# Kernel tuning notes

Hardware: AMD Instinct MI355X
Metric: run time of the kernel (lower is better)

Reference implementation:

```python
import jax, jax.numpy as jnp
import numpy as np

D_MODEL = 1024
N_HEADS = 16
D_HEAD = D_MODEL // N_HEADS


def setup_inputs() -> dict:
    key = jax.random.key(0)
    k1, k2, k3 = jax.random.split(key, 3)
    x = jax.random.normal(k1, (2, 2048, D_MODEL), dtype=jnp.float32)
    # torch Linear weights transposed to [in, out] for x @ W
    w_qkv = jax.random.normal(k2, (D_MODEL, 3 * D_MODEL), dtype=jnp.float32) * (D_MODEL ** -0.5)
    w_proj = jax.random.normal(k3, (D_MODEL, D_MODEL), dtype=jnp.float32) * (D_MODEL ** -0.5)
    return {"x": x, "w_qkv": w_qkv, "w_proj": w_proj}


def reference(x, w_qkv, w_proj):
    B, N, D = x.shape
    qkv = x @ w_qkv                              # [B, N, 3D]
    q, k, v = jnp.split(qkv, 3, axis=-1)         # each [B, N, D]

    def split_heads(t):
        return t.reshape(B, N, N_HEADS, D_HEAD).transpose(0, 2, 1, 3)  # [B, H, N, d]

    q, k, v = map(split_heads, (q, k, v))
    scale = 1.0 / jnp.sqrt(jnp.float32(D_HEAD))
    scores = jnp.einsum('bhnd,bhmd->bhnm', q, k) * scale   # [B, H, N, N]
    attn = jax.nn.softmax(scores, axis=-1)
    out = jnp.einsum('bhnm,bhmd->bhnd', attn, v)            # [B, H, N, d]
    out = out.transpose(0, 2, 1, 3).reshape(B, N, D)        # merge heads
    return out @ w_proj + x
```

## Files before the change

### kernel.cpp

```cpp
#include <hip/hip_runtime.h>
#include <hip/hip_bf16.h>
#include <cstdint>
#include <cstddef>

typedef __bf16 bf16;
typedef __attribute__((ext_vector_type(4))) float f32x4;
typedef __attribute__((ext_vector_type(16))) float f32x16;
typedef __attribute__((ext_vector_type(8))) __bf16 bf16x8;
typedef __attribute__((ext_vector_type(4))) __bf16 bf16x4;
typedef __attribute__((ext_vector_type(4))) unsigned int u32x4;

#define D_MODEL 1024
#define NHEADS  16
#define DHEAD   64
#define SEQ     2048
#define BATCH   2
#define MROWS   (BATCH*SEQ)
#define BHTOT   (BATCH*NHEADS)

#define QSCALE 0.18033688011112042f
#define DEFER_THR 11.5f

__device__ __forceinline__ void gload16(const bf16* g, bf16* l) {
  __builtin_amdgcn_global_load_lds(
      (const __attribute__((address_space(1))) void*)g,
      (__attribute__((address_space(3))) void*)l, 16, 0, 0);
}

__device__ __forceinline__ f32x4 mfma16(bf16x8 a, bf16x8 b, f32x4 c) {
  return __builtin_amdgcn_mfma_f32_16x16x32_bf16(a, b, c, 0, 0, 0);
}

__device__ __forceinline__ f32x16 mfma32(bf16x8 a, bf16x8 b, f32x16 c) {
  return __builtin_amdgcn_mfma_f32_32x32x16_bf16(a, b, c, 0, 0, 0);
}

__device__ __forceinline__ float fexp2(float x) {
#if __has_builtin(__builtin_amdgcn_exp2f)
  return __builtin_amdgcn_exp2f(x);
#else
  float r; asm("v_exp_f32 %0, %1" : "=v"(r) : "v"(x)); return r;
#endif
}

__device__ __forceinline__ unsigned cvtpk(float lo, float hi) {
  unsigned r;
  asm("v_cvt_pk_bf16_f32 %0, %1, %2" : "=v"(r) : "v"(lo), "v"(hi));
  return r;
}


__global__ void cast_f32_bf16(const float* __restrict__ in, bf16* __restrict__ out, int n4) {
  int i = blockIdx.x * blockDim.x + threadIdx.x;
  if (i >= n4) return;
  float4 v = ((const float4*)in)[i];
  bf16x4 o;
  o[0] = (bf16)v.x; o[1] = (bf16)v.y; o[2] = (bf16)v.z; o[3] = (bf16)v.w;
  ((bf16x4*)out)[i] = o;
}

__global__ void tcast(const float* __restrict__ in, bf16* __restrict__ out, int R, int C) {
  __shared__ float t[32][33];
  int c0 = blockIdx.x * 32, r0 = blockIdx.y * 32;
  int tx = threadIdx.x, ty = threadIdx.y;
  #pragma unroll
  for (int i = 0; i < 4; i++)
    t[ty + i*8][tx] = in[(size_t)(r0 + ty + i*8) * C + c0 + tx];
  __syncthreads();
  #pragma unroll
  for (int i = 0; i < 4; i++)
    out[(size_t)(c0 + ty + i*8) * R + r0 + tx] = (bf16)t[tx][ty + i*8];
}


template <int EPI>
__global__ __launch_bounds__(256, 3) void gemm_bt(
    const bf16* __restrict__ A, const bf16* __restrict__ Bt, int K, int N,
    bf16* __restrict__ qb, bf16* __restrict__ kb, bf16* __restrict__ vtb,
    const float* __restrict__ xres, float* __restrict__ outf) {
  __shared__ alignas(16) bf16 As[128 * 64];
  __shared__ alignas(16) bf16 Bs[128 * 64];
  const int tid = threadIdx.x;
  const int wave = tid >> 6, lane = tid & 63;
  const int wr = wave >> 1, wc = wave & 1;
  const int m0 = blockIdx.y * 128, n0 = blockIdx.x * 128;
  const int srow = lane >> 3;
  const int scol = ((lane & 7) ^ srow) * 8;
  const int lr16 = lane & 15, lg = lane >> 4;
  const int rsw = (lr16 & 7) << 4;
  const int cA = (lg * 16) ^ rsw;
  const int cB = (64 + lg * 16) ^ rsw;
  const char* aP = (const char*)As + (wr*64 + lr16) * 128;
  const char* bP = (const char*)Bs + (wc*64 + lr16) * 128;

  f32x4 acc[4][4];
  #pragma unroll
  for (int m = 0; m < 4; m++)
    #pragma unroll
    for (int n = 0; n < 4; n++) acc[m][n] = (f32x4)0.0f;

  for (int k0 = 0; k0 < K; k0 += 64) {
    #pragma unroll
    for (int j = 0; j < 4; j++) {
      const int c = wave * 4 + j;
      gload16(A  + (size_t)(m0 + c*8 + srow) * K + k0 + scol, &As[c * 512]);
      gload16(Bt + (size_t)(n0 + c*8 + srow) * K + k0 + scol, &Bs[c * 512]);
    }
    __syncthreads();
    bf16x8 af[4][2], bfr[4][2];
    #pragma unroll
    for (int m = 0; m < 4; m++) {
      af[m][0] = *(const bf16x8*)(aP + m*2048 + cA);
      af[m][1] = *(const bf16x8*)(aP + m*2048 + cB);
    }
    #pragma unroll
    for (int n = 0; n < 4; n++) {
      bfr[n][0] = *(const bf16x8*)(bP + n*2048 + cA);
      bfr[n][1] = *(const bf16x8*)(bP + n*2048 + cB);
    }
    #pragma unroll
    for (int m = 0; m < 4; m++)
      #pragma unroll
      for (int n = 0; n < 4; n++) {
        acc[m][n] = mfma16(af[m][0], bfr[n][0], acc[m][n]);
        acc[m][n] = mfma16(af[m][1], bfr[n][1], acc[m][n]);
      }
    __syncthreads();
  }

  #pragma unroll
  for (int n = 0; n < 4; n++) {
    const int colg = n0 + wc*64 + n*16 + lr16;
    if (EPI == 0) {
      const int which = colg >> 10;
      const int win = colg & 1023;
      const int h = win >> 6, d = win & 63;
      #pragma unroll
      for (int m = 0; m < 4; m++) {
        const int rowg0 = m0 + wr*64 + m*16 + lg*4;
        #pragma unroll
        for (int j = 0; j < 4; j++) {
          const int rowg = rowg0 + j;
          const int b = rowg >> 11, r = rowg & 2047;
          const int bh = (b << 4) + h;
          if (which == 2) {
            vtb[((size_t)bh * DHEAD + d) * SEQ + r] = (bf16)acc[m][n][j];
          } else {
            bf16* dst = (which == 0) ? qb : kb;
            const float sc = (which == 0) ? QSCALE : 1.0f;
            dst[((size_t)bh * SEQ + r) * DHEAD + d] = (bf16)(acc[m][n][j] * sc);
          }
        }
      }
    } else {
      #pragma unroll
      for (int m = 0; m < 4; m++) {
        const int rowg0 = m0 + wr*64 + m*16 + lg*4;
        #pragma unroll
        for (int j = 0; j < 4; j++) {
          const size_t idx = (size_t)(rowg0 + j) * N + colg;
          outf[idx] = acc[m][n][j] + xres[idx];
        }
      }
    }
  }
}

__global__ __launch_bounds__(256, 2) void attn_kernel(
    const bf16* __restrict__ q, const bf16* __restrict__ k,
    const bf16* __restrict__ vt, bf16* __restrict__ o) {
  __shared__ alignas(16) bf16 Ks[2][64 * 64];
  __shared__ alignas(16) bf16 Vs[2][64 * 64];
  const int tid = threadIdx.x;
  const int wave = tid >> 6, lane = tid & 63;
  const int l31 = lane & 31, hi = lane >> 5;
  const int bh = blockIdx.y;
  const int b = bh >> 4, h = bh & 15;
  const int qr = blockIdx.x * 128 + wave * 32;
  const bf16* kh = k  + (size_t)bh * SEQ * DHEAD;
  const bf16* vh = vt + (size_t)bh * DHEAD * SEQ;

  const int srow = lane >> 3;
  const int scol = ((lane & 7) ^ srow) * 8;
  const bf16* kg = kh + (size_t)(wave*16 + srow) * DHEAD + scol;
  const bf16* vg = vh + (size_t)(wave*16 + srow) * SEQ + scol;
  bf16* ldsK0 = &Ks[0][wave * 1024];
  bf16* ldsK1 = &Ks[1][wave * 1024];
  bf16* ldsV0 = &Vs[0][wave * 1024];
  bf16* ldsV1 = &Vs[1][wave * 1024];

  const bf16* qrow = q + (size_t)bh * SEQ * DHEAD + (size_t)(qr + l31) * DHEAD;
  bf16x8 qf[4];
  #pragma unroll
  for (int ks = 0; ks < 4; ks++)
    qf[ks] = *(const bf16x8*)&qrow[ks * 16 + hi * 8];

  float mr = 0.0f, lsum = 0.0f;
  f32x16 acc0 = (f32x16)0.0f, acc1 = (f32x16)0.0f;

  const int rsw = (lane & 7) << 4;
  const int rowoff = l31 * 128;
  int cofs[4];
  #pragma unroll
  for (int ks = 0; ks < 4; ks++) cofs[ks] = (ks * 32 + hi * 16) ^ rsw;
  const char* kr0 = (const char*)&Ks[0][0] + rowoff;
  const char* kr1 = (const char*)&Ks[1][0] + rowoff;
  const char* vr0 = (const char*)&Vs[0][0] + rowoff;
  const char* vr1 = (const char*)&Vs[1][0] + rowoff;

  gload16(kg, ldsK0); gload16(kg + 8 * DHEAD, ldsK0 + 512);
  gload16(vg, ldsV0); gload16(vg + 8 * SEQ,   ldsV0 + 512);
  kg += 64 * DHEAD; vg += 64;
  __syncthreads();

  const int NT = SEQ / 64;
  for (int t = 0; t < NT; ++t) {
    bf16* dK = (t & 1) ? ldsK0 : ldsK1;
    bf16* dV = (t & 1) ? ldsV0 : ldsV1;
    if (t + 1 < NT) {
      gload16(kg, dK); gload16(kg + 8 * DHEAD, dK + 512);
      gload16(vg, dV); gload16(vg + 8 * SEQ,   dV + 512);
      kg += 64 * DHEAD; vg += 64;
    }
    const char* kr = (t & 1) ? kr1 : kr0;
    const char* vr = (t & 1) ? vr1 : vr0;

    #pragma unroll
    for (int th = 0; th < 2; ++th) {
      const int toff = th * 4096;

      const float nmr = -mr;
      f32x16 s = (f32x16)nmr;
      __builtin_amdgcn_s_setprio(1);
      #pragma unroll
      for (int ks = 0; ks < 4; ks++) {
        bf16x8 kf = *(const bf16x8*)(kr + toff + cofs[ks]);
        s = mfma32(kf, qf[ks], s);
      }
      __builtin_amdgcn_s_setprio(0);

      const float a0 = fmaxf(fmaxf(s[0], s[1]), fmaxf(s[2], s[3]));
      const float a1 = fmaxf(fmaxf(s[4], s[5]), fmaxf(s[6], s[7]));
      const float a2 = fmaxf(fmaxf(s[8], s[9]), fmaxf(s[10], s[11]));
      const float a3 = fmaxf(fmaxf(s[12], s[13]), fmaxf(s[14], s[15]));
      const float lmax = fmaxf(fmaxf(a0, a1), fmaxf(a2, a3));

      if (!__all(lmax <= DEFER_THR)) {
        float mx = fmaxf(lmax, __shfl_xor(lmax, 32));
        mx = fmaxf(mx, 0.0f);
        const float corr = fexp2(-mx);
        lsum *= corr;
        acc0 *= corr; acc1 *= corr;
        mr += mx;
        #pragma unroll
        for (int r = 0; r < 16; r++) s[r] -= mx;
      }

      #pragma unroll
      for (int r = 0; r < 16; r++) s[r] = fexp2(s[r]);
      lsum += (((s[0] + s[1]) + (s[2] + s[3])) + ((s[4] + s[5]) + (s[6] + s[7])))
            + (((s[8] + s[9]) + (s[10] + s[11])) + ((s[12] + s[13]) + (s[14] + s[15])));

      __builtin_amdgcn_s_setprio(1);
      #pragma unroll
      for (int u = 0; u < 2; ++u) {
        const unsigned w0 = cvtpk(s[8*u + 0], s[8*u + 1]);
        const unsigned w1 = cvtpk(s[8*u + 2], s[8*u + 3]);
        const unsigned w2 = cvtpk(s[8*u + 4], s[8*u + 5]);
        const unsigned w3 = cvtpk(s[8*u + 6], s[8*u + 7]);
        const unsigned p0 = (unsigned)__shfl_xor((int)w0, 32);
        const unsigned p1 = (unsigned)__shfl_xor((int)w1, 32);
        const unsigned p2 = (unsigned)__shfl_xor((int)w2, 32);
        const unsigned p3 = (unsigned)__shfl_xor((int)w3, 32);
        u32x4 fw;
        fw[0] = hi ? p2 : w0;
        fw[1] = hi ? p3 : w1;
        fw[2] = hi ? w2 : p0;
        fw[3] = hi ? w3 : p1;
        bf16x8 pf = __builtin_bit_cast(bf16x8, fw);
        const int ksl = 2 * th + u;
        bf16x8 vf0 = *(const bf16x8*)(vr + cofs[ksl]);
        bf16x8 vf1 = *(const bf16x8*)(vr + 4096 + cofs[ksl]);
        acc0 = mfma32(vf0, pf, acc0);
        acc1 = mfma32(vf1, pf, acc1);
      }
      __builtin_amdgcn_s_setprio(0);
    }

    __syncthreads();
  }

  lsum += __shfl_xor(lsum, 32);
  const float inv = 1.0f / lsum;
  bf16* orow = o + ((size_t)(b * SEQ + qr + l31)) * D_MODEL + h * 64 + hi * 4;
  #pragma unroll
  for (int g = 0; g < 4; g++) {
    bf16x4 o0, o1;
    #pragma unroll
    for (int e = 0; e < 4; e++) {
      o0[e] = (bf16)(acc0[4*g + e] * inv);
      o1[e] = (bf16)(acc1[4*g + e] * inv);
    }
    *(bf16x4*)&orow[8 * g]      = o0;
    *(bf16x4*)&orow[32 + 8 * g] = o1;
  }
}


extern "C" void kernel_launch(void* const* d_in, const int* in_sizes, int n_in,
                              void* d_out, int out_size, void* d_ws, size_t ws_size,
                              hipStream_t stream) {
  const float* x      = (const float*)d_in[0];
  const float* w_qkv  = (const float*)d_in[1];
  const float* w_proj = (const float*)d_in[2];
  float* outf = (float*)d_out;

  bf16* xb    = (bf16*)d_ws;
  bf16* wqkvT = xb    + (size_t)MROWS * D_MODEL;
  bf16* wpT   = wqkvT + (size_t)3 * D_MODEL * D_MODEL;
  bf16* qb    = wpT   + (size_t)D_MODEL * D_MODEL;
  bf16* kb    = qb    + (size_t)BHTOT * SEQ * DHEAD;
  bf16* vtb   = kb    + (size_t)BHTOT * SEQ * DHEAD;
  bf16* ob    = xb;

  dim3 tb(32, 8);

  cast_f32_bf16<<<(MROWS * D_MODEL / 4 + 255) / 256, 256, 0, stream>>>(
      x, xb, MROWS * D_MODEL / 4);
  tcast<<<dim3(3 * D_MODEL / 32, D_MODEL / 32), tb, 0, stream>>>(
      w_qkv, wqkvT, D_MODEL, 3 * D_MODEL);
  tcast<<<dim3(D_MODEL / 32, D_MODEL / 32), tb, 0, stream>>>(
      w_proj, wpT, D_MODEL, D_MODEL);

  gemm_bt<0><<<dim3(3 * D_MODEL / 128, MROWS / 128), 256, 0, stream>>>(
      xb, wqkvT, D_MODEL, 3 * D_MODEL, qb, kb, vtb, nullptr, nullptr);

  attn_kernel<<<dim3(SEQ / 128, BHTOT), 256, 0, stream>>>(qb, kb, vtb, ob);

  gemm_bt<1><<<dim3(D_MODEL / 128, MROWS / 128), 256, 0, stream>>>(
      ob, wpT, D_MODEL, D_MODEL, nullptr, nullptr, nullptr, x, outf);
}
```

Baseline: 139.2 us.

## Split KV sequence across two wave groups per attention block and merge in LDS

The attention block grows from 4 to 8 waves. The two groups of 4 waves each process half of the key/value sequence for the same 128 query rows, using separate double-buffered LDS regions. At the end, the second group writes its partial accumulators, running max and sum to LDS. The first group then rescales both partials with the online-softmax merge and writes the output. The aim is to halve the serial KV loop per block and double resident waves for better latency hiding. The cost is a tighter register budget from launch bounds of 512, plus 64KB of LDS per block.

After: 134.9 us. 3.1% less time.

```diff
diff --git a/kernel.cpp b/kernel.cpp
--- a/kernel.cpp
+++ b/kernel.cpp
@@ -166,28 +166,31 @@
   }
 }
 
-__global__ __launch_bounds__(256, 2) void attn_kernel(
+__global__ __launch_bounds__(512, 2) void attn_kernel(
     const bf16* __restrict__ q, const bf16* __restrict__ k,
     const bf16* __restrict__ vt, bf16* __restrict__ o) {
-  __shared__ alignas(16) bf16 Ks[2][64 * 64];
-  __shared__ alignas(16) bf16 Vs[2][64 * 64];
+  __shared__ alignas(16) char smraw[65536];
+  bf16* kvb = (bf16*)smraw;
+  float* mg = (float*)smraw;
+
   const int tid = threadIdx.x;
   const int wave = tid >> 6, lane = tid & 63;
+  const int qw = wave & 3, kh2 = wave >> 2;
   const int l31 = lane & 31, hi = lane >> 5;
   const int bh = blockIdx.y;
   const int b = bh >> 4, h = bh & 15;
-  const int qr = blockIdx.x * 128 + wave * 32;
+  const int qr = blockIdx.x * 128 + qw * 32;
   const bf16* kh = k  + (size_t)bh * SEQ * DHEAD;
   const bf16* vh = vt + (size_t)bh * DHEAD * SEQ;
 
   const int srow = lane >> 3;
   const int scol = ((lane & 7) ^ srow) * 8;
-  const bf16* kg = kh + (size_t)(wave*16 + srow) * DHEAD + scol;
-  const bf16* vg = vh + (size_t)(wave*16 + srow) * SEQ + scol;
-  bf16* ldsK0 = &Ks[0][wave * 1024];
-  bf16* ldsK1 = &Ks[1][wave * 1024];
-  bf16* ldsV0 = &Vs[0][wave * 1024];
-  bf16* ldsV1 = &Vs[1][wave * 1024];
+  const bf16* kg = kh + (size_t)(kh2 * 1024 + qw * 16 + srow) * DHEAD + scol;
+  const bf16* vg = vh + (size_t)(qw * 16 + srow) * SEQ + kh2 * 1024 + scol;
+  bf16* ldsK0 = kvb + kh2 * 16384 +        qw * 1024;
+  bf16* ldsK1 = kvb + kh2 * 16384 + 8192 + qw * 1024;
+  bf16* ldsV0 = kvb + kh2 * 16384 + 4096 +        qw * 1024;
+  bf16* ldsV1 = kvb + kh2 * 16384 + 8192 + 4096 + qw * 1024;
 
   const bf16* qrow = q + (size_t)bh * SEQ * DHEAD + (size_t)(qr + l31) * DHEAD;
   bf16x8 qf[4];
@@ -203,17 +206,17 @@
   int cofs[4];
   #pragma unroll
   for (int ks = 0; ks < 4; ks++) cofs[ks] = (ks * 32 + hi * 16) ^ rsw;
-  const char* kr0 = (const char*)&Ks[0][0] + rowoff;
-  const char* kr1 = (const char*)&Ks[1][0] + rowoff;
-  const char* vr0 = (const char*)&Vs[0][0] + rowoff;
-  const char* vr1 = (const char*)&Vs[1][0] + rowoff;
+  const char* kr0 = (const char*)(kvb + kh2 * 16384) + rowoff;
+  const char* kr1 = (const char*)(kvb + kh2 * 16384 + 8192) + rowoff;
+  const char* vr0 = (const char*)(kvb + kh2 * 16384 + 4096) + rowoff;
+  const char* vr1 = (const char*)(kvb + kh2 * 16384 + 8192 + 4096) + rowoff;
 
   gload16(kg, ldsK0); gload16(kg + 8 * DHEAD, ldsK0 + 512);
   gload16(vg, ldsV0); gload16(vg + 8 * SEQ,   ldsV0 + 512);
   kg += 64 * DHEAD; vg += 64;
   __syncthreads();
 
-  const int NT = SEQ / 64;
+  const int NT = 1024 / 64;
   for (int t = 0; t < NT; ++t) {
     bf16* dK = (t & 1) ? ldsK0 : ldsK1;
     bf16* dV = (t & 1) ? ldsV0 : ldsV1;
@@ -291,18 +294,36 @@
   }
 
   lsum += __shfl_xor(lsum, 32);
-  const float inv = 1.0f / lsum;
-  bf16* orow = o + ((size_t)(b * SEQ + qr + l31)) * D_MODEL + h * 64 + hi * 4;
-  #pragma unroll
-  for (int g = 0; g < 4; g++) {
-    bf16x4 o0, o1;
-    #pragma unroll
-    for (int e = 0; e < 4; e++) {
-      o0[e] = (bf16)(acc0[4*g + e] * inv);
-      o1[e] = (bf16)(acc1[4*g + e] * inv);
-    }
-    *(bf16x4*)&orow[8 * g]      = o0;
-    *(bf16x4*)&orow[32 + 8 * g] = o1;
+
+  if (kh2 == 1) {
+    float* dst = &mg[(qw * 64 + lane) * 35];
+    #pragma unroll
+    for (int r = 0; r < 16; r++) dst[r] = acc0[r];
+    #pragma unroll
+    for (int r = 0; r < 16; r++) dst[16 + r] = acc1[r];
+    dst[32] = lsum; dst[33] = mr;
+  }
+  __syncthreads();
+  if (kh2 == 0) {
+    const float* src = &mg[(qw * 64 + lane) * 35];
+    const float lsb = src[32], mrb = src[33];
+    const float M  = fmaxf(mr, mrb);
+    const float wa = fexp2(mr - M), wb = fexp2(mrb - M);
+    const float inv = 1.0f / (lsum * wa + lsb * wb);
+    const float fa = wa * inv, fb = wb * inv;
+
+    bf16* orow = o + ((size_t)(b * SEQ + qr + l31)) * D_MODEL + h * 64 + hi * 4;
+    #pragma unroll
+    for (int g = 0; g < 4; g++) {
+      bf16x4 o0, o1;
+      #pragma unroll
+      for (int e = 0; e < 4; e++) {
+        o0[e] = (bf16)(acc0[4*g + e] * fa + src[4*g + e] * fb);
+        o1[e] = (bf16)(acc1[4*g + e] * fa + src[16 + 4*g + e] * fb);
+      }
+      *(bf16x4*)&orow[8 * g]      = o0;
+      *(bf16x4*)&orow[32 + 8 * g] = o1;
+    }
   }
 }
 
@@ -335,7 +356,7 @@
   gemm_bt<0><<<dim3(3 * D_MODEL / 128, MROWS / 128), 256, 0, stream>>>(
       xb, wqkvT, D_MODEL, 3 * D_MODEL, qb, kb, vtb, nullptr, nullptr);
 
-  attn_kernel<<<dim3(SEQ / 128, BHTOT), 256, 0, stream>>>(qb, kb, vtb, ob);
+  attn_kernel<<<dim3(SEQ / 128, BHTOT), 512, 0, stream>>>(qb, kb, vtb, ob);
 
   gemm_bt<1><<<dim3(D_MODEL / 128, MROWS / 128), 256, 0, stream>>>(
       ob, wpT, D_MODEL, D_MODEL, nullptr, nullptr, nullptr, x, outf);
```
